# Kernel optimization log

Hardware: AMD Instinct MI355X
Metric: run time of the kernel (lower is better)

Reference implementation:

```python
import jax, jax.numpy as jnp
import numpy as np
from jax import lax

B, N, E = 256, 100_000, 3_200_000
VOCAB, EMB, FT, DIM, OUT = 65, 128, 41, 32, 128
BN_EPS = 1e-5


def setup_inputs() -> dict:
    key = jax.random.key(0)
    ks = jax.random.split(key, 40)
    f = lambda i, shape: jax.random.normal(ks[i], shape, jnp.float32) * 0.05
    inp = {
        'xd': jax.random.randint(ks[0], (B, 100), 0, VOCAB),
        'xt': jax.random.normal(ks[1], (N, FT), jnp.float32),
        'edge_index': jax.random.randint(ks[2], (2, E), 0, N),
        'batch': jnp.sort(jax.random.randint(ks[3], (N,), 0, B)),
        'y': jax.random.normal(ks[4], (B,), jnp.float32),
        # drug branch params
        'emb': f(5, (VOCAB, EMB)),
        'conv_w': f(6, (32, 100, 8)),   # OIH for Conv1d(100->32, k=8)
        'conv_b': f(7, (32,)),
        'fcd_w': f(8, (32 * 121, OUT)),
        'fcd_b': f(9, (OUT,)),
        # GIN layer 1 MLP (41->32->32)
        'g1_w1': f(10, (FT, DIM)), 'g1_b1': f(11, (DIM,)),
        'g1_w2': f(12, (DIM, DIM)), 'g1_b2': f(13, (DIM,)),
        # GIN layers 2-5 MLPs (32->32->32), stacked
        'gw1': f(14, (4, DIM, DIM)), 'gb1': f(15, (4, DIM)),
        'gw2': f(16, (4, DIM, DIM)), 'gb2': f(17, (4, DIM)),
        # BatchNorm (eval mode running stats) for 5 layers
        'bn_g': f(18, (5, DIM)) + 1.0,
        'bn_b': f(19, (5, DIM)),
        'bn_rm': f(20, (5, DIM)),
        'bn_rv': jax.random.uniform(ks[21], (5, DIM), jnp.float32, 0.5, 1.5),
        # protein fc + classifier
        'fct_w': f(22, (DIM, OUT)), 'fct_b': f(23, (OUT,)),
        'c1_w': f(24, (256, 1024)), 'c1_b': f(25, (1024,)),
        'c2_w': f(26, (1024, 256)), 'c2_b': f(27, (256,)),
        'c3_w': f(28, (256, 1)), 'c3_b': f(29, (1,)),
    }
    return inp


def reference(xd, xt, edge_index, batch, y, emb, conv_w, conv_b, fcd_w, fcd_b,
              g1_w1, g1_b1, g1_w2, g1_b2, gw1, gb1, gw2, gb2,
              bn_g, bn_b, bn_rm, bn_rv, fct_w, fct_b,
              c1_w, c1_b, c2_w, c2_b, c3_w, c3_b):
    # ---- drug branch ----
    e = emb[xd]                                        # [B, 100, 128]
    c = lax.conv_general_dilated(e, conv_w, (1,), 'VALID',
                                 dimension_numbers=('NCH', 'OIH', 'NCH'))
    c = c + conv_b[None, :, None]                      # [B, 32, 121]
    xd_f = c.reshape(B, 32 * 121) @ fcd_w + fcd_b      # [B, 128]

    src, dst = edge_index[0], edge_index[1]
    h = xt
    for i in range(5):
        agg = h + jax.ops.segment_sum(h[src], dst, num_segments=N)
        if i == 0:
            w1, b1, w2, b2 = g1_w1, g1_b1, g1_w2, g1_b2
        else:
            w1, b1, w2, b2 = gw1[i - 1], gb1[i - 1], gw2[i - 1], gb2[i - 1]
        h = jax.nn.relu(agg @ w1 + b1) @ w2 + b2       # GIN MLP
        h = jax.nn.relu(h)                              # F.relu after conv
        h = bn_g[i] * (h - bn_rm[i]) * lax.rsqrt(bn_rv[i] + BN_EPS) + bn_b[i]
    pooled = jax.ops.segment_sum(h, batch, num_segments=B)  # global_add_pool
    xt_f = jax.nn.relu(pooled @ fct_w + fct_b)         # dropout = identity (eval)

    # ---- classifier ----
    xj = jnp.concatenate([xd_f, xt_f], axis=1)         # [B, 256]
    h1 = jax.nn.relu(xj @ c1_w + c1_b)
    h2 = jax.nn.relu(h1 @ c2_w + c2_b)
    out = (h2 @ c3_w + c3_b).squeeze(1)                # [B]
    return out, y
```

## Files before the change

### kernel.cpp

```cpp
#include <hip/hip_runtime.h>

typedef unsigned int u32;
typedef unsigned char u8;

#define NN 100000
#define NE 3200000
#define NB 256
#define FTD 41
#define DIM 32
#define NBK 782
#define SCHUNK 8000

typedef __fp16 fp16x2 __attribute__((ext_vector_type(2)));

__device__ __forceinline__ float h16f(u32 bits) {
  union { unsigned short s; _Float16 h; } c;
  c.s = (unsigned short)bits;
  return (float)c.h;
}
__device__ __forceinline__ u32 pk2(float a, float b) {
  union { fp16x2 h; u32 u; } c;
  c.h = __builtin_amdgcn_cvt_pkrtz(a, b);
  return c.u;
}

__device__ __forceinline__ u8 f8enc(float v) {
  union { _Float16 h; unsigned short u; } cv;
  cv.h = (_Float16)(v * 0.00390625f);
  u32 h = cv.u;
  u32 mag = h & 0x7fffu;
  u32 base = mag >> 7;
  u32 low = mag & 0x7fu;
  base += (low > 0x40u || (low == 0x40u && (base & 1u))) ? 1u : 0u;
  if (base > 0x7eu) base = 0x7eu;
  return (u8)(((h >> 8) & 0x80u) | base);
}

__device__ __forceinline__ void acc4(u32 w, float* a) {
#pragma unroll
  for (int i = 0; i < 4; i++) {
    u32 bb = (w >> (8 * i)) & 0xffu;
    a[i] += h16f(((bb & 0x80u) << 8) | ((bb & 0x7fu) << 7));
  }
}
__device__ __forceinline__ void accrow(uint4 r0, uint4 r1, float* acc) {
  acc4(r0.x, acc + 0);  acc4(r0.y, acc + 4);
  acc4(r0.z, acc + 8);  acc4(r0.w, acc + 12);
  acc4(r1.x, acc + 16); acc4(r1.y, acc + 20);
  acc4(r1.z, acc + 24); acc4(r1.w, acc + 28);
}

__global__ __launch_bounds__(256) void k_bzero(int* __restrict__ bcnt) {
  int g = blockIdx.x * 256 + threadIdx.x;
  if (g < NBK) bcnt[g] = 0;
}

__global__ __launch_bounds__(256) void k_bhist(const int* __restrict__ ei,
                                               int* __restrict__ bcnt) {
  __shared__ int h[NBK];
  int t = threadIdx.x;
  for (int i = t; i < NBK; i += 256) h[i] = 0;
  __syncthreads();
  for (int g = blockIdx.x * 256 + t; g < NE; g += gridDim.x * 256)
    atomicAdd(&h[ei[NE + g] >> 7], 1);
  __syncthreads();
  for (int i = t; i < NBK; i += 256)
    if (h[i]) atomicAdd(&bcnt[i], h[i]);
}

__global__ __launch_bounds__(1024) void k_bscan(const int* __restrict__ bcnt,
                                                int* __restrict__ boff,
                                                int* __restrict__ bcur) {
  __shared__ int sm[1024];
  int t = threadIdx.x;
  int v = (t < NBK) ? bcnt[t] : 0;
  sm[t] = v;
  __syncthreads();
  for (int d = 1; d < 1024; d <<= 1) {
    int x = (t >= d) ? sm[t - d] : 0;
    __syncthreads();
    sm[t] += x;
    __syncthreads();
  }
  if (t < NBK) {
    int excl = sm[t] - v;
    boff[t] = excl;
    bcur[t] = excl;
  }
  if (t == 0) boff[NBK] = NE;
}

__global__ __launch_bounds__(256) void k_bscatter(const int* __restrict__ ei,
                                                  int* __restrict__ bcur,
                                                  int* __restrict__ ppack) {
  __shared__ int lexcl[NBK];
  __shared__ int lcur[NBK];
  __shared__ int gdelta[NBK];
  __shared__ int lbuf[SCHUNK];
  __shared__ unsigned short lbkt[SCHUNK];
  __shared__ int sm[256];
  int t = threadIdx.x;
  int e0 = blockIdx.x * SCHUNK;
  for (int i = t; i < NBK; i += 256) lexcl[i] = 0;
  __syncthreads();
  for (int i = t; i < SCHUNK; i += 256)
    atomicAdd(&lexcl[((u32)ei[NE + e0 + i]) >> 7], 1);
  __syncthreads();
  int b0 = t * 4;
  int c0 = 0, c1 = 0, c2 = 0, c3 = 0;
  if (b0 < NBK) {
    c0 = lexcl[b0];
    c1 = (b0 + 1 < NBK) ? lexcl[b0 + 1] : 0;
    c2 = (b0 + 2 < NBK) ? lexcl[b0 + 2] : 0;
    c3 = (b0 + 3 < NBK) ? lexcl[b0 + 3] : 0;
  }
  int tot = c0 + c1 + c2 + c3;
  sm[t] = tot;
  __syncthreads();
  for (int d = 1; d < 256; d <<= 1) {
    int x = (t >= d) ? sm[t - d] : 0;
    __syncthreads();
    sm[t] += x;
    __syncthreads();
  }
  int base = sm[t] - tot;
  if (b0 < NBK) {
    int cnts[4] = {c0, c1, c2, c3};
    int e = base;
#pragma unroll
    for (int j = 0; j < 4; j++) {
      int b = b0 + j;
      if (b < NBK) {
        int c = cnts[j];
        lexcl[b] = e;
        lcur[b] = e;
        if (c > 0) gdelta[b] = atomicAdd(&bcur[b], c) - e;
        e += c;
      }
    }
  }
  __syncthreads();
  for (int i = t; i < SCHUNK; i += 256) {
    int s = ei[e0 + i];
    u32 d = (u32)ei[NE + e0 + i];
    int b = d >> 7;
    int p = atomicAdd(&lcur[b], 1);
    lbuf[p] = (int)(((d & 127u) << 20) | (u32)s);
    lbkt[p] = (unsigned short)b;
  }
  __syncthreads();
  for (int i = t; i < SCHUNK; i += 256) {
    int b = lbkt[i];
    ppack[gdelta[b] + i] = lbuf[i];
  }
}

__global__ __launch_bounds__(256) void k_bfinal(const int* __restrict__ boff,
                                                const int* __restrict__ ppack,
                                                int* __restrict__ off,
                                                int* __restrict__ srcs) {
  __shared__ int ncnt[128];
  __shared__ int nincl[128];
  int b = blockIdx.x, t = threadIdx.x;
  int e0 = boff[b], e1 = boff[b + 1];
  if (t < 128) ncnt[t] = 0;
  __syncthreads();
  for (int i = e0 + t; i < e1; i += 256) atomicAdd(&ncnt[((u32)ppack[i]) >> 20], 1);
  __syncthreads();
  if (t < 128) nincl[t] = ncnt[t];
  __syncthreads();
  for (int d = 1; d < 128; d <<= 1) {
    int x = 0;
    if (t < 128 && t >= d) x = nincl[t - d];
    __syncthreads();
    if (t < 128) nincl[t] += x;
    __syncthreads();
  }
  int node0 = b * 128;
  if (t < 128) {
    int excl = nincl[t] - ncnt[t];
    int node = node0 + t;
    if (node < NN) off[node] = e0 + excl;
    ncnt[t] = excl;
  }
  if (b == 0 && t == 0) off[NN] = NE;
  __syncthreads();
  for (int i = e0 + t; i < e1; i += 256) {
    u32 v = (u32)ppack[i];
    int dl = v >> 20;
    int pos = atomicAdd(&ncnt[dl], 1);
    srcs[e0 + pos] = (int)(v & 0xFFFFF);
  }
}

__global__ __launch_bounds__(256) void k_conv(
    const int* __restrict__ xd, const float* __restrict__ emb,
    const float* __restrict__ convw, const float* __restrict__ convb,
    float* __restrict__ C) {
  __shared__ float e_s[50 * 132 + 16];
  __shared__ float w_s[4 * 800];
  __shared__ int xd_s[100];
  int t = threadIdx.x;
  int b = blockIdx.x >> 3;
  int og = (blockIdx.x & 7) << 2;
  if (t < 100) xd_s[t] = xd[b * 100 + t];
  for (int i = t; i < 3200; i += 256) w_s[i] = convw[og * 800 + i];
  int ol = t >> 6;
  int ht = t & 63;
  int h0 = ht * 2;
  float a0 = 0.f, a1 = 0.f;
  const float4* wv = (const float4*)&w_s[ol * 800];
  for (int c = 0; c < 2; c++) {
    __syncthreads();
    for (int idx = t; idx < 6400; idx += 256) {
      int ch = idx >> 7, pos = idx & 127;
      e_s[ch * 132 + pos] = emb[xd_s[c * 50 + ch] * 128 + pos];
    }
    __syncthreads();
    for (int i = 0; i < 50; i++) {
      const float2* ep2 = (const float2*)&e_s[i * 132 + h0];
      float2 v0 = ep2[0], v1 = ep2[1], v2 = ep2[2], v3 = ep2[3], v4 = ep2[4];
      int ci = c * 50 + i;
      float4 wa = wv[ci * 2], wb = wv[ci * 2 + 1];
      a0 += v0.x * wa.x + v0.y * wa.y + v1.x * wa.z + v1.y * wa.w +
            v2.x * wb.x + v2.y * wb.y + v3.x * wb.z + v3.y * wb.w;
      a1 += v0.y * wa.x + v1.x * wa.y + v1.y * wa.z + v2.x * wa.w +
            v2.y * wb.x + v3.x * wb.y + v3.y * wb.z + v4.x * wb.w;
    }
  }
  int o = og + ol;
  float bb = convb[o];
  float* cp = &C[b * 3872 + o * 121];
  if (h0 < 121) cp[h0] = a0 + bb;
  if (h0 + 1 < 121) cp[h0 + 1] = a1 + bb;
}

__global__ __launch_bounds__(256) void k_fcd(
    const float* __restrict__ C, const float* __restrict__ fcdw,
    const float* __restrict__ fcdb, float* __restrict__ XJ) {
  __shared__ float c_s[3872];
  __shared__ float red[128];
  int t = threadIdx.x, b = blockIdx.x;
  for (int i = t; i < 3872; i += 256) c_s[i] = C[b * 3872 + i];
  __syncthreads();
  int j = t & 127, half = t >> 7;
  float acc = 0.f;
  int k0 = half * 1936;
  for (int k = k0; k < k0 + 1936; k++) acc += c_s[k] * fcdw[k * 128 + j];
  if (half) red[j] = acc;
  __syncthreads();
  if (!half) XJ[b * 256 + j] = acc + red[j] + fcdb[j];
}

__global__ __launch_bounds__(256) void k_z1(
    const float* __restrict__ xt, const float* __restrict__ w1,
    u8* __restrict__ Z, float* __restrict__ pool) {
  __shared__ float xs[256 * FTD];
  __shared__ float w1s[FTD * DIM];
  int t = threadIdx.x;
  int base = blockIdx.x * 256;
  int g = base + t;
  if (g < NB * DIM) pool[g] = 0.f;
  for (int i = t; i < FTD * DIM; i += 256) w1s[i] = w1[i];
  int cnt = min(256, NN - base);
  for (int i = t; i < cnt * FTD; i += 256) xs[i] = xt[base * FTD + i];
  __syncthreads();
  int n = base + t;
  if (n < NN) {
    float acc[DIM];
#pragma unroll
    for (int j = 0; j < DIM; j++) acc[j] = 0.f;
    for (int k = 0; k < FTD; k++) {
      float xk = xs[t * FTD + k];
#pragma unroll
      for (int j = 0; j < DIM; j++) acc[j] += xk * w1s[k * DIM + j];
    }
    u8* zp = &Z[n * DIM];
#pragma unroll
    for (int j = 0; j < DIM; j++) zp[j] = f8enc(acc[j]);
  }
}

template <int HAS_NEXT, int DO_POOL>
__global__ __launch_bounds__(256) void k_gin(
    const int* __restrict__ off, const int* __restrict__ srcs,
    const u8* __restrict__ Zin, const float* __restrict__ b1,
    const float* __restrict__ w2, const float* __restrict__ b2,
    const float* __restrict__ bng, const float* __restrict__ bnb,
    const float* __restrict__ bnrm, const float* __restrict__ bnrv,
    const float* __restrict__ w1n, u8* __restrict__ Zout,
    float* __restrict__ pool, const int* __restrict__ batch) {
  __shared__ float w2s[DIM * DIM];
  __shared__ float w1ns[DIM * DIM];
  __shared__ u32 aggs[256 * 17];
  int t = threadIdx.x;
  for (int i = t; i < DIM * DIM; i += 256) {
    w2s[i] = w2[i];
    if (HAS_NEXT) w1ns[i] = w1n[i];
  }
  int m = t >> 3, p = t & 7;
  int n = blockIdx.x * 32 + m;
  {
    float acc[DIM];
#pragma unroll
    for (int i = 0; i < DIM; i++) acc[i] = 0.f;
    int beg = off[n], end = off[n + 1];
    if (p == 0) {
      const uint4* zr = (const uint4*)(Zin + n * DIM);
      uint4 r0 = zr[0], r1 = zr[1];
      accrow(r0, r1, acc);
    }
    int j = beg + p;
    for (; j + 8 < end; j += 16) {
      int sA = srcs[j], sB = srcs[j + 8];
      const uint4* ra = (const uint4*)(Zin + sA * DIM);
      const uint4* rb = (const uint4*)(Zin + sB * DIM);
      uint4 a0 = ra[0], a1 = ra[1];
      uint4 c0 = rb[0], c1 = rb[1];
      accrow(a0, a1, acc);
      accrow(c0, c1, acc);
    }
    if (j < end) {
      int sA = srcs[j];
      const uint4* ra = (const uint4*)(Zin + sA * DIM);
      uint4 a0 = ra[0], a1 = ra[1];
      accrow(a0, a1, acc);
    }
#pragma unroll
    for (int q = 0; q < 16; q++)
      aggs[t * 17 + q] = pk2(acc[2 * q], acc[2 * q + 1]);
  }
  __syncthreads();
  int g = t >> 5, f = t & 31;
  float b1f = b1[f], b2f = b2[f];
  float sc = bng[f] * rsqrtf(bnrv[f] + 1e-5f);
  float sh = bnb[f] - bnrm[f] * sc;
  int w = f >> 1, hi = f & 1;
#pragma unroll 1
  for (int mm = 0; mm < 4; mm++) {
    int lm = g * 4 + mm;
    int node = blockIdx.x * 32 + lm;
    int s8 = lm * 8;
    float agg = 0.f;
#pragma unroll
    for (int q = 0; q < 8; q++) {
      u32 u = aggs[(s8 + q) * 17 + w];
      agg += h16f(hi ? (u >> 16) : (u & 0xffffu));
    }
    agg *= 256.0f;
    float hid = fmaxf(agg + b1f, 0.f);
    float o = b2f;
#pragma unroll
    for (int k = 0; k < DIM; k++) o += __shfl(hid, k, 32) * w2s[k * DIM + f];
    float hn = fmaxf(o, 0.f) * sc + sh;
    if (HAS_NEXT) {
      float z = 0.f;
#pragma unroll
      for (int k = 0; k < DIM; k++) z += __shfl(hn, k, 32) * w1ns[k * DIM + f];
      Zout[node * DIM + f] = f8enc(z);
    }
    if (DO_POOL) atomicAdd(&pool[batch[node] * DIM + f], hn);
  }
}

__global__ __launch_bounds__(128) void k_fct(
    const float* __restrict__ pool, const float* __restrict__ fctw,
    const float* __restrict__ fctb, float* __restrict__ XJ) {
  __shared__ float p_s[DIM];
  int t = threadIdx.x, b = blockIdx.x;
  if (t < DIM) p_s[t] = pool[b * DIM + t];
  __syncthreads();
  float acc = fctb[t];
  for (int k = 0; k < DIM; k++) acc += p_s[k] * fctw[k * 128 + t];
  XJ[b * 256 + 128 + t] = fmaxf(acc, 0.f);
}

__global__ __launch_bounds__(256) void k_c1(
    const float* __restrict__ XJ, const float* __restrict__ w,
    const float* __restrict__ bias, float* __restrict__ H1) {
  __shared__ float xs[256];
  int t = threadIdx.x, b = blockIdx.y;
  xs[t] = XJ[b * 256 + t];
  __syncthreads();
  int j = blockIdx.x * 256 + t;
  float acc = bias[j];
  for (int k = 0; k < 256; k++) acc += xs[k] * w[k * 1024 + j];
  H1[b * 1024 + j] = fmaxf(acc, 0.f);
}

__global__ __launch_bounds__(256) void k_c2(
    const float* __restrict__ H1, const float* __restrict__ w,
    const float* __restrict__ bias, float* __restrict__ H2) {
  __shared__ float hs[1024];
  int t = threadIdx.x, b = blockIdx.x;
  for (int i = t; i < 1024; i += 256) hs[i] = H1[b * 1024 + i];
  __syncthreads();
  float acc = bias[t];
  for (int k = 0; k < 1024; k++) acc += hs[k] * w[k * 256 + t];
  H2[b * 256 + t] = fmaxf(acc, 0.f);
}

__global__ __launch_bounds__(64) void k_c3(
    const float* __restrict__ H2, const float* __restrict__ w,
    const float* __restrict__ bias, const float* __restrict__ y,
    float* __restrict__ out) {
  int b = blockIdx.x * 64 + threadIdx.x;
  float acc = bias[0];
  for (int k = 0; k < 256; k++) acc += H2[b * 256 + k] * w[k];
  out[b] = acc;
  out[NB + b] = y[b];
}

extern "C" void kernel_launch(void* const* d_in, const int* in_sizes, int n_in,
                              void* d_out, int out_size, void* d_ws,
                              size_t ws_size, hipStream_t stream) {
  const int* xd = (const int*)d_in[0];
  const float* xt = (const float*)d_in[1];
  const int* ei = (const int*)d_in[2];
  const int* batch = (const int*)d_in[3];
  const float* y = (const float*)d_in[4];
  const float* emb = (const float*)d_in[5];
  const float* convw = (const float*)d_in[6];
  const float* convb = (const float*)d_in[7];
  const float* fcdw = (const float*)d_in[8];
  const float* fcdb = (const float*)d_in[9];
  const float* g1w1 = (const float*)d_in[10];
  const float* g1b1 = (const float*)d_in[11];
  const float* g1w2 = (const float*)d_in[12];
  const float* g1b2 = (const float*)d_in[13];
  const float* gw1 = (const float*)d_in[14];
  const float* gb1 = (const float*)d_in[15];
  const float* gw2 = (const float*)d_in[16];
  const float* gb2 = (const float*)d_in[17];
  const float* bng = (const float*)d_in[18];
  const float* bnb = (const float*)d_in[19];
  const float* bnrm = (const float*)d_in[20];
  const float* bnrv = (const float*)d_in[21];
  const float* fctw = (const float*)d_in[22];
  const float* fctb = (const float*)d_in[23];
  const float* c1w = (const float*)d_in[24];
  const float* c1b = (const float*)d_in[25];
  const float* c2w = (const float*)d_in[26];
  const float* c2b = (const float*)d_in[27];
  const float* c3w = (const float*)d_in[28];
  const float* c3b = (const float*)d_in[29];
  float* out = (float*)d_out;

  u8* Z0 = (u8*)d_ws;
  u8* Z1 = Z0 + (size_t)NN * DIM;
  int* srcs = (int*)(Z1 + (size_t)NN * DIM);
  int* off = srcs + NE;
  int* bcnt = off + NN + 1;
  int* boff = bcnt + NBK;
  int* bcur = boff + NBK + 1;
  int* ppack = bcur + NBK;
  float* C = (float*)ppack;
  float* XJ = C + (size_t)NB * 3872;
  float* H1 = XJ + NB * 256;
  float* H2 = H1 + NB * 1024;
  float* POOL = H2 + NB * 256;

  int nblk = (NN + 255) / 256;
  int gblk = NN / 32;

  k_bzero<<<(NBK + 255) / 256, 256, 0, stream>>>(bcnt);
  k_bhist<<<512, 256, 0, stream>>>(ei, bcnt);
  k_bscan<<<1, 1024, 0, stream>>>(bcnt, boff, bcur);
  k_bscatter<<<NE / SCHUNK, 256, 0, stream>>>(ei, bcur, ppack);
  k_bfinal<<<NBK, 256, 0, stream>>>(boff, ppack, off, srcs);

  k_conv<<<NB * 8, 256, 0, stream>>>(xd, emb, convw, convb, C);
  k_fcd<<<NB, 256, 0, stream>>>(C, fcdw, fcdb, XJ);

  k_z1<<<nblk, 256, 0, stream>>>(xt, g1w1, Z0, POOL);
  u8* zin = Z0;
  u8* zout = Z1;
  for (int i = 0; i < 5; i++) {
    const float *b1, *w2, *b2;
    if (i == 0) { b1 = g1b1; w2 = g1w2; b2 = g1b2; }
    else {
      b1 = gb1 + (i - 1) * DIM;
      w2 = gw2 + (i - 1) * DIM * DIM;
      b2 = gb2 + (i - 1) * DIM;
    }
    const float* w1n = gw1 + i * DIM * DIM;
    if (i < 4)
      k_gin<1, 0><<<gblk, 256, 0, stream>>>(
          off, srcs, zin, b1, w2, b2, bng + i * DIM, bnb + i * DIM,
          bnrm + i * DIM, bnrv + i * DIM, w1n, zout, POOL, batch);
    else
      k_gin<0, 1><<<gblk, 256, 0, stream>>>(
          off, srcs, zin, b1, w2, b2, bng + i * DIM, bnb + i * DIM,
          bnrm + i * DIM, bnrv + i * DIM, w1n, zout, POOL, batch);
    u8* tmp = zin; zin = zout; zout = tmp;
  }
  k_fct<<<NB, 128, 0, stream>>>(POOL, fctw, fctb, XJ);
  k_c1<<<dim3(4, NB), 256, 0, stream>>>(XJ, c1w, c1b, H1);
  k_c2<<<NB, 256, 0, stream>>>(H1, c2w, c2b, H2);
  k_c3<<<4, 64, 0, stream>>>(H2, c3w, c3b, y, out);
}
```

Before: 685.7 us.

## Aggregate GIN neighbors with one thread per node and vectorized index loads

The GIN aggregation used to split each node's neighbor list across 8 threads and then reduce their fp16 partial sums through shared memory. Now one thread owns a whole node, walks its CSR edge list with aligned int4 index loads, and issues four row gathers per iteration. Blocks shrink to 128 threads, and the MLP phase reads a single aggregated row per node. This removes the cross-thread reduction and cuts index-load instructions, but each thread now runs a long serial loop (about 32 edges), which lowers parallelism per node and may lead to divergence when degrees are uneven.

```diff
diff --git a/kernel.cpp b/kernel.cpp
--- a/kernel.cpp
+++ b/kernel.cpp
@@ -282,7 +282,7 @@
 }
 
 template <int HAS_NEXT, int DO_POOL>
-__global__ __launch_bounds__(256) void k_gin(
+__global__ __launch_bounds__(128) void k_gin(
     const int* __restrict__ off, const int* __restrict__ srcs,
     const u8* __restrict__ Zin, const float* __restrict__ b1,
     const float* __restrict__ w2, const float* __restrict__ b2,
@@ -292,39 +292,45 @@
     float* __restrict__ pool, const int* __restrict__ batch) {
   __shared__ float w2s[DIM * DIM];
   __shared__ float w1ns[DIM * DIM];
-  __shared__ u32 aggs[256 * 17];
+  __shared__ u32 aggs[128 * 17];
   int t = threadIdx.x;
-  for (int i = t; i < DIM * DIM; i += 256) {
+  for (int i = t; i < DIM * DIM; i += 128) {
     w2s[i] = w2[i];
     if (HAS_NEXT) w1ns[i] = w1n[i];
   }
-  int m = t >> 3, p = t & 7;
-  int n = blockIdx.x * 32 + m;
-  {
+  int n = blockIdx.x * 128 + t;
+  if (n < NN) {
     float acc[DIM];
 #pragma unroll
     for (int i = 0; i < DIM; i++) acc[i] = 0.f;
+    const uint4* zr = (const uint4*)(Zin + n * DIM);
+    accrow(zr[0], zr[1], acc);
     int beg = off[n], end = off[n + 1];
-    if (p == 0) {
-      const uint4* zr = (const uint4*)(Zin + n * DIM);
-      uint4 r0 = zr[0], r1 = zr[1];
+    int j = beg;
+    for (; j < end && (j & 3); j++) {
+      const uint4* r = (const uint4*)(Zin + srcs[j] * DIM);
+      uint4 r0 = r[0], r1 = r[1];
       accrow(r0, r1, acc);
     }
-    int j = beg + p;
-    for (; j + 8 < end; j += 16) {
-      int sA = srcs[j], sB = srcs[j + 8];
-      const uint4* ra = (const uint4*)(Zin + sA * DIM);
-      const uint4* rb = (const uint4*)(Zin + sB * DIM);
-      uint4 a0 = ra[0], a1 = ra[1];
-      uint4 c0 = rb[0], c1 = rb[1];
-      accrow(a0, a1, acc);
-      accrow(c0, c1, acc);
-    }
-    if (j < end) {
-      int sA = srcs[j];
-      const uint4* ra = (const uint4*)(Zin + sA * DIM);
-      uint4 a0 = ra[0], a1 = ra[1];
-      accrow(a0, a1, acc);
+    for (; j + 4 <= end; j += 4) {
+      int4 s4 = *(const int4*)&srcs[j];
+      const uint4* rx = (const uint4*)(Zin + s4.x * DIM);
+      const uint4* ry = (const uint4*)(Zin + s4.y * DIM);
+      const uint4* rz = (const uint4*)(Zin + s4.z * DIM);
+      const uint4* rw = (const uint4*)(Zin + s4.w * DIM);
+      uint4 x0 = rx[0], x1 = rx[1];
+      uint4 y0 = ry[0], y1 = ry[1];
+      uint4 z0 = rz[0], z1 = rz[1];
+      uint4 w0 = rw[0], w1 = rw[1];
+      accrow(x0, x1, acc);
+      accrow(y0, y1, acc);
+      accrow(z0, z1, acc);
+      accrow(w0, w1, acc);
+    }
+    for (; j < end; j++) {
+      const uint4* r = (const uint4*)(Zin + srcs[j] * DIM);
+      uint4 r0 = r[0], r1 = r[1];
+      accrow(r0, r1, acc);
     }
 #pragma unroll
     for (int q = 0; q < 16; q++)
@@ -337,17 +343,12 @@
   float sh = bnb[f] - bnrm[f] * sc;
   int w = f >> 1, hi = f & 1;
 #pragma unroll 1
-  for (int mm = 0; mm < 4; mm++) {
-    int lm = g * 4 + mm;
-    int node = blockIdx.x * 32 + lm;
-    int s8 = lm * 8;
-    float agg = 0.f;
-#pragma unroll
-    for (int q = 0; q < 8; q++) {
-      u32 u = aggs[(s8 + q) * 17 + w];
-      agg += h16f(hi ? (u >> 16) : (u & 0xffffu));
-    }
-    agg *= 256.0f;
+  for (int mm = 0; mm < 32; mm++) {
+    int lm = g * 32 + mm;
+    int node = blockIdx.x * 128 + lm;
+    if (node >= NN) break;
+    u32 u = aggs[lm * 17 + w];
+    float agg = h16f(hi ? (u >> 16) : (u & 0xffffu)) * 256.0f;
     float hid = fmaxf(agg + b1f, 0.f);
     float o = b2f;
 #pragma unroll
@@ -461,7 +462,7 @@
   float* POOL = H2 + NB * 256;
 
   int nblk = (NN + 255) / 256;
-  int gblk = NN / 32;
+  int gblk = (NN + 127) / 128;
 
   k_bzero<<<(NBK + 255) / 256, 256, 0, stream>>>(bcnt);
   k_bhist<<<512, 256, 0, stream>>>(ei, bcnt);
@@ -485,11 +486,11 @@
     }
     const float* w1n = gw1 + i * DIM * DIM;
     if (i < 4)
-      k_gin<1, 0><<<gblk, 256, 0, stream>>>(
+      k_gin<1, 0><<<gblk, 128, 0, stream>>>(
           off, srcs, zin, b1, w2, b2, bng + i * DIM, bnb + i * DIM,
           bnrm + i * DIM, bnrv + i * DIM, w1n, zout, POOL, batch);
     else
-      k_gin<0, 1><<<gblk, 256, 0, stream>>>(
+      k_gin<0, 1><<<gblk, 128, 0, stream>>>(
           off, srcs, zin, b1, w2, b2, bng + i * DIM, bnb + i * DIM,
           bnrm + i * DIM, bnrv + i * DIM, w1n, zout, POOL, batch);
     u8* tmp = zin; zin = zout; zout = tmp;
```

New measurement: 847.2 us. +23.6%, slower.
